# Kernel optimization log

Measured on AMD Instinct MI355X. Metric: run time of the kernel, lower is better.

The kernel has to match this reference:

```python
import jax, jax.numpy as jnp
from jax import lax
import numpy as np

B, N, S, K, C = 8, 16384, 1024, 32, 256


def setup_inputs() -> dict:
    key = jax.random.key(0)
    ks = jax.random.split(key, 8)
    def lin(k, o, i):
        return (jax.random.normal(k, (o, i), jnp.float32) / np.sqrt(i)).astype(jnp.float32)
    return {
        "x": jax.random.normal(ks[0], (B, N, 3), jnp.float32),
        "Wqkv": lin(ks[1], 3 * C, 3), "bqkv": jnp.zeros((3 * C,), jnp.float32),
        "g1": lin(ks[2], C, C), "bg1": jnp.zeros((C,), jnp.float32),
        "g2": lin(ks[3], C, C), "bg2": jnp.zeros((C,), jnp.float32),
        "Wo": lin(ks[4], C, C), "bo": jnp.zeros((C,), jnp.float32),
        "p1": lin(ks[5], 128, 3), "bp1": jnp.zeros((128,), jnp.float32),
        "p2": lin(ks[6], C, 128), "bp2": jnp.zeros((C,), jnp.float32),
    }


def _fps(xyz, num_patches):
    # furthest point sampling, deterministic start at index 0 (matches pointnet2 CUDA op)
    b, n, _ = xyz.shape
    def body(carry, _):
        dmin, far = carry
        c = jnp.take_along_axis(xyz, far[:, None, None], axis=1)[:, 0]  # [B,3]
        d = jnp.sum((xyz - c[:, None, :]) ** 2, axis=-1)                # [B,N]
        dmin = jnp.minimum(dmin, d)
        return (dmin, jnp.argmax(dmin, axis=-1)), far
    init = (jnp.full((b, n), 1e10, xyz.dtype), jnp.zeros((b,), jnp.int32))
    _, idx = lax.scan(body, init, None, length=num_patches)
    return jnp.transpose(idx)  # [B,S]


def _gelu(x):
    return jax.nn.gelu(x, approximate=False)  # torch nn.GELU default = exact erf


def reference(x, Wqkv, bqkv, g1, bg1, g2, bg2, Wo, bo, p1, bp1, p2, bp2):
    scale = C ** (-0.5)
    fps_idx = _fps(x, S)                                        # [B,S]
    centroid = jnp.take_along_axis(x, fps_idx[..., None], axis=1)  # [B,S,3]
    # square_distance(centroid, x): [B,S,N]
    d = (jnp.sum(centroid ** 2, -1)[..., None]
         + jnp.sum(x ** 2, -1)[:, None, :]
         - 2.0 * jnp.einsum('bsc,bnc->bsn', centroid, x))
    _, knn = lax.top_k(-d, K)                                   # [B,S,K] smallest-k (== argsort[:, :, :k])
    grouped = jax.vmap(lambda pts, i: pts[i])(x, knn)           # [B,S,K,3]
    # 1x1 Conv2d over channel dim == linear on last axis
    qkv = grouped @ Wqkv.T + bqkv                               # [B,S,K,3C]
    q, k_, v = jnp.split(qkv, 3, axis=-1)
    q = q.max(axis=2); k_ = k_.max(axis=2); v = v.max(axis=2)   # [B,S,C]
    h = _gelu((q - k_) @ g1.T + bg1) @ g2.T + bg2               # fc_gamma MLP
    attn = jax.nn.softmax(h * scale, axis=-1)                   # softmax over channels
    pos = _gelu(centroid @ p1.T + bp1) @ p2.T + bp2             # [B,S,C]
    return (attn * v) @ Wo.T + bo + pos                         # [B,S,C]
```

## Files before the change

### kernel.cpp

```cpp
#include <hip/hip_runtime.h>
#include <hip/hip_bf16.h>
#include <cstdint>

#define B_ 8
#define N_ 16384
#define S_ 1024
#define K_ 32
#define C_ 256
#define RR 8

typedef float vf16 __attribute__((ext_vector_type(16)));
typedef float vf8  __attribute__((ext_vector_type(8)));
typedef float vf4  __attribute__((ext_vector_type(4)));

__device__ __forceinline__ float gelu_f(float x){
  return 0.5f * x * (1.0f + erff(x * 0.70710678118654752f));
}

__device__ __forceinline__ float dist2_f(float px, float py, float pz,
                                         float cx, float cy, float cz){
  float dx = px - cx, dy = py - cy, dz = pz - cz;
  return dx*dx + dy*dy + dz*dz;
}

__global__ void prep_kernel(const float* __restrict__ x,
                            const float* __restrict__ g1,
                            const float* __restrict__ g2,
                            const float* __restrict__ Wo,
                            const float* __restrict__ p2,
                            float* __restrict__ xT,
                            float* __restrict__ g1T,
                            float* __restrict__ g2T,
                            float* __restrict__ WoT,
                            float* __restrict__ p2T,
                            float4* __restrict__ xP){
  int u = blockIdx.x * 256 + threadIdx.x;
  if (u < B_*N_){
    int b = u >> 14, n = u & (N_-1);
    const float* p = x + (size_t)u * 3;
    float X = p[0], Y = p[1], Z = p[2];
    xT[((size_t)b*3+0)*N_ + n] = X;
    xT[((size_t)b*3+1)*N_ + n] = Y;
    xT[((size_t)b*3+2)*N_ + n] = Z;
    xP[u] = make_float4(X, Y, Z, 0.0f);
  } else if (u < B_*N_ + 65536){
    int v = u - B_*N_; int i = v >> 8, j = v & 255;
    g1T[v] = g1[j*256 + i];
  } else if (u < B_*N_ + 2*65536){
    int v = u - B_*N_ - 65536; int i = v >> 8, j = v & 255;
    g2T[v] = g2[j*256 + i];
  } else if (u < B_*N_ + 3*65536){
    int v = u - B_*N_ - 2*65536; int i = v >> 8, j = v & 255;
    WoT[v] = Wo[j*256 + i];
  } else if (u < B_*N_ + 3*65536 + 32768){
    int v = u - B_*N_ - 3*65536; int i = v >> 8, j = v & 255;
    p2T[v] = p2[j*128 + i];
  }
}

__global__ __launch_bounds__(512, 1) void fps_kernel(const float4* __restrict__ xP,
                                                     float* __restrict__ cent){
  int b = blockIdx.x;
  int tid = threadIdx.x;
  const float4* P = xP + (size_t)b * N_;
  vf16 px0, py0, pz0, px1, py1, pz1;
  #pragma unroll
  for (int i=0;i<16;i++){
    float4 p = P[i*512 + tid];
    px0[i]=p.x; py0[i]=p.y; pz0[i]=p.z;
  }
  #pragma unroll
  for (int i=0;i<16;i++){
    float4 p = P[(i+16)*512 + tid];
    px1[i]=p.x; py1[i]=p.y; pz1[i]=p.z;
  }
  vf16 dm0 = (vf16)1e10f, dm1 = (vf16)1e10f;
  __shared__ float wmax[8];
  __shared__ int islot[2];
  __shared__ float centb[S_*3];
  if (tid < 2) islot[tid] = 0x7FFFFFFF;
  __syncthreads();
  float4 c4 = P[0];
  for (int s=0; s<S_; s++){
    int cur = s & 1;
    if (tid == 0){
      centb[s*3+0]=c4.x; centb[s*3+1]=c4.y; centb[s*3+2]=c4.z;
    }
    float cx=c4.x, cy=c4.y, cz=c4.z;
    {
      vf16 dx = px0 - cx, dy = py0 - cy, dz = pz0 - cz;
      vf16 d  = dx*dx + dy*dy + dz*dz;
      dm0 = __builtin_elementwise_min(dm0, d);
    }
    {
      vf16 dx = px1 - cx, dy = py1 - cy, dz = pz1 - cz;
      vf16 d  = dx*dx + dy*dy + dz*dz;
      dm1 = __builtin_elementwise_min(dm1, d);
    }
    vf16 mm = __builtin_elementwise_max(dm0, dm1);
    vf8 m8 = __builtin_elementwise_max(
        __builtin_shufflevector(mm, mm, 0,1,2,3,4,5,6,7),
        __builtin_shufflevector(mm, mm, 8,9,10,11,12,13,14,15));
    vf4 m4 = __builtin_elementwise_max(
        __builtin_shufflevector(m8, m8, 0,1,2,3),
        __builtin_shufflevector(m8, m8, 4,5,6,7));
    float wm = fmaxf(fmaxf(m4.x,m4.y), fmaxf(m4.z,m4.w));
    #pragma unroll
    for (int off=32; off; off>>=1) wm = fmaxf(wm, __shfl_xor(wm, off));
    if ((tid & 63) == 0) wmax[tid>>6] = wm;
    __syncthreads();
    if (tid == 0) islot[cur^1] = 0x7FFFFFFF;
    float g0 = fmaxf(fmaxf(wmax[0],wmax[1]), fmaxf(wmax[2],wmax[3]));
    float g1v = fmaxf(fmaxf(wmax[4],wmax[5]), fmaxf(wmax[6],wmax[7]));
    float gm = fmaxf(g0, g1v);
    if (wm == gm){
      int cidx = 0x7FFFFFFF;
      #pragma unroll
      for (int i=15;i>=0;i--){ if (dm1[i]==gm) cidx = (i+16)*512 + tid; }
      #pragma unroll
      for (int i=15;i>=0;i--){ if (dm0[i]==gm) cidx = i*512 + tid; }
      if (cidx != 0x7FFFFFFF) atomicMin(&islot[cur], cidx);
    }
    __syncthreads();
    int far = islot[cur];
    c4 = P[far];
  }
  __syncthreads();
  for (int i = tid; i < S_*3; i += 512) cent[(size_t)b*S_*3 + i] = centb[i];
}

__global__ __launch_bounds__(256) void knn_qkv_kernel(const float* __restrict__ xT,
                                                      const float* __restrict__ cent,
                                                      const float* __restrict__ Wqkv,
                                                      const float* __restrict__ bqkv,
                                                      float* __restrict__ qkv){
  __shared__ unsigned hist[RR][256];
  __shared__ unsigned candB[RR][256];
  __shared__ int      candI[RR][256];
  __shared__ int      selI[RR][32];
  __shared__ float    pts[RR][32][3];
  __shared__ int      cnt[RR];
  __shared__ int      Bstar[RR];
  int tid = threadIdx.x;
  int row0 = blockIdx.x * RR;
  int b = row0 >> 10;
  const float* X = xT + (size_t)b*3*N_;
  const float* Y = X + N_;
  const float* Z = Y + N_;
  float cx[RR], cy[RR], cz[RR];
  #pragma unroll
  for (int r=0;r<RR;r++){
    const float* c = cent + ((size_t)row0 + r)*3;
    cx[r]=c[0]; cy[r]=c[1]; cz[r]=c[2];
  }
  for (int i=tid; i<RR*256; i+=256) ((unsigned*)hist)[i] = 0u;
  if (tid < RR) cnt[tid]=0;
  __syncthreads();
  for (int i=0;i<64;i++){
    int g = i*256 + tid;
    float px=X[g], py=Y[g], pz=Z[g];
    #pragma unroll
    for (int r=0;r<RR;r++){
      float d = dist2_f(px,py,pz,cx[r],cy[r],cz[r]);
      int key = (int)(__float_as_uint(d) >> 20) - 840;
      key = min(max(key,0),255);
      atomicAdd(&hist[r][key], 1u);
    }
  }
  __syncthreads();
  int w = tid >> 6, lane = tid & 63;
  for (int half=0; half<2; half++){
    int r = half*4 + w;
    uint4 h4 = ((uint4*)&hist[r][0])[lane];
    unsigned cum = h4.x + h4.y + h4.z + h4.w;
    for (int off=1; off<64; off<<=1){
      unsigned t = __shfl_up(cum, off);
      if (lane >= off) cum += t;
    }
    unsigned long long mask = __ballot(cum >= 32u);
    int lb = __ffsll((unsigned long long)mask) - 1;
    unsigned cumPrev = __shfl(cum, lb>0 ? lb-1 : 0);
    if (lane == lb){
      unsigned c0 = (lb==0) ? 0u : cumPrev;
      unsigned hh[4] = {h4.x,h4.y,h4.z,h4.w};
      int bs = lb*4 + 3;
      for (int k=0;k<4;k++){
        if (c0 + hh[k] >= 32u){ bs = lb*4 + k; break; }
        c0 += hh[k];
      }
      Bstar[r] = bs;
    }
  }
  __syncthreads();
  int bsr[RR];
  #pragma unroll
  for (int r=0;r<RR;r++) bsr[r] = min(Bstar[r]+1, 255);
  for (int i=0;i<64;i++){
    int g = i*256 + tid;
    float px=X[g], py=Y[g], pz=Z[g];
    #pragma unroll
    for (int r=0;r<RR;r++){
      float d = dist2_f(px,py,pz,cx[r],cy[r],cz[r]);
      unsigned bits = __float_as_uint(d);
      int key = min(max((int)(bits>>20) - 840, 0), 255);
      if (key <= bsr[r]){
        int pos = atomicAdd(&cnt[r], 1);
        if (pos < 256){ candB[r][pos] = bits; candI[r][pos] = g; }
      }
    }
  }
  __syncthreads();
  for (int half=0; half<2; half++){
    int r = half*4 + w;
    int L = min(cnt[r], 256);
    for (int j=lane; j<L; j+=64){
      unsigned mb = candB[r][j]; int mi = candI[r][j];
      int rank = 0;
      for (int t=0;t<L;t++){
        unsigned tb = candB[r][t]; int ti = candI[r][t];
        rank += (tb < mb || (tb == mb && ti < mi)) ? 1 : 0;
      }
      if (rank < 32) selI[r][rank] = mi;
    }
  }
  __syncthreads();
  { int r = tid >> 5, p = tid & 31;
    int g = selI[r][p];
    pts[r][p][0]=X[g]; pts[r][p][1]=Y[g]; pts[r][p][2]=Z[g]; }
  __syncthreads();
  float w0[3], w1[3], w2[3], bb[3];
  #pragma unroll
  for (int c3=0;c3<3;c3++){
    int c = tid + c3*256;
    w0[c3]=Wqkv[c*3+0]; w1[c3]=Wqkv[c*3+1]; w2[c3]=Wqkv[c*3+2]; bb[c3]=bqkv[c];
  }
  for (int r=0;r<RR;r++){
    float m0=-1e30f, m1=-1e30f, m2=-1e30f;
    #pragma unroll
    for (int p=0;p<32;p++){
      float px=pts[r][p][0], py=pts[r][p][1], pz=pts[r][p][2];
      m0 = fmaxf(m0, w0[0]*px + w1[0]*py + w2[0]*pz);
      m1 = fmaxf(m1, w0[1]*px + w1[1]*py + w2[1]*pz);
      m2 = fmaxf(m2, w0[2]*px + w1[2]*py + w2[2]*pz);
    }
    float* o = qkv + ((size_t)row0 + r)*768;
    o[tid      ] = m0 + bb[0];
    o[tid + 256] = m1 + bb[1];
    o[tid + 512] = m2 + bb[2];
  }
}

template<int KD>
__device__ __forceinline__ void gemm_tile(const float* A_, const float* __restrict__ Wt,
                                          int rb, int lane, float acc[4][4]){
  const float4* W4 = (const float4*)Wt;
  for (int i0=0; i0<(KD>>2); i0++){
    float4 wv0 = W4[(i0*4+0)*64 + lane];
    float4 wv1 = W4[(i0*4+1)*64 + lane];
    float4 wv2 = W4[(i0*4+2)*64 + lane];
    float4 wv3 = W4[(i0*4+3)*64 + lane];
    #pragma unroll
    for (int r=0;r<4;r++){
      float4 a = ((const float4*)(A_ + (size_t)(rb+r)*KD))[i0];
      acc[r][0] = fmaf(a.x,wv0.x,fmaf(a.y,wv1.x,fmaf(a.z,wv2.x,fmaf(a.w,wv3.x,acc[r][0]))));
      acc[r][1] = fmaf(a.x,wv0.y,fmaf(a.y,wv1.y,fmaf(a.z,wv2.y,fmaf(a.w,wv3.y,acc[r][1]))));
      acc[r][2] = fmaf(a.x,wv0.z,fmaf(a.y,wv1.z,fmaf(a.z,wv2.z,fmaf(a.w,wv3.z,acc[r][2]))));
      acc[r][3] = fmaf(a.x,wv0.w,fmaf(a.y,wv1.w,fmaf(a.z,wv2.w,fmaf(a.w,wv3.w,acc[r][3]))));
    }
  }
}

__global__ __launch_bounds__(512, 2) void stage2_kernel(const float* __restrict__ qkv,
                                                        const float* __restrict__ cent,
                                                        const float* __restrict__ g1T,
                                                        const float* __restrict__ bg1,
                                                        const float* __restrict__ g2T,
                                                        const float* __restrict__ bg2,
                                                        const float* __restrict__ WoT,
                                                        const float* __restrict__ bo,
                                                        const float* __restrict__ p1,
                                                        const float* __restrict__ bp1,
                                                        const float* __restrict__ p2T,
                                                        const float* __restrict__ bp2,
                                                        float* __restrict__ out){
  __shared__ float A[32][256];
  __shared__ float T[32][128];
  __shared__ float CC[32][3];
  int tid = threadIdx.x;
  int w = tid >> 6, lane = tid & 63;
  int rb = w * 4;
  int row0 = blockIdx.x * 32;
  const float4* qkv4 = (const float4*)qkv;
  #pragma unroll
  for (int t=0;t<4;t++){
    int fi = t*512 + tid;
    int r = fi >> 6, c4 = fi & 63;
    float4 q = qkv4[(size_t)(row0+r)*192 + c4];
    float4 k = qkv4[(size_t)(row0+r)*192 + 64 + c4];
    ((float4*)&A[r][0])[c4] = make_float4(q.x-k.x, q.y-k.y, q.z-k.z, q.w-k.w);
  }
  if (tid < 96) ((float*)CC)[tid] = cent[(size_t)row0*3 + tid];
  __syncthreads();
  #pragma unroll
  for (int t=0;t<8;t++){
    int e = t*512 + tid;
    int r = e >> 7, c = e & 127;
    float tv = CC[r][0]*p1[c*3+0] + CC[r][1]*p1[c*3+1] + CC[r][2]*p1[c*3+2] + bp1[c];
    T[r][c] = gelu_f(tv);
  }
  __syncthreads();
  float acc[4][4];
  #pragma unroll
  for (int r=0;r<4;r++){ acc[r][0]=0.f; acc[r][1]=0.f; acc[r][2]=0.f; acc[r][3]=0.f; }
  gemm_tile<256>(&A[0][0], g1T, rb, lane, acc);
  {
    float4 bg = ((const float4*)bg1)[lane];
    #pragma unroll
    for (int r=0;r<4;r++){
      float4 g;
      g.x = gelu_f(acc[r][0] + bg.x);
      g.y = gelu_f(acc[r][1] + bg.y);
      g.z = gelu_f(acc[r][2] + bg.z);
      g.w = gelu_f(acc[r][3] + bg.w);
      ((float4*)&A[rb+r][0])[lane] = g;
    }
  }
  #pragma unroll
  for (int r=0;r<4;r++){ acc[r][0]=0.f; acc[r][1]=0.f; acc[r][2]=0.f; acc[r][3]=0.f; }
  gemm_tile<256>(&A[0][0], g2T, rb, lane, acc);
  {
    float4 bg = ((const float4*)bg2)[lane];
    const float scale = 0.0625f;
    #pragma unroll
    for (int r=0;r<4;r++){
      float h0 = acc[r][0]+bg.x, h1 = acc[r][1]+bg.y, h2 = acc[r][2]+bg.z, h3 = acc[r][3]+bg.w;
      float mx = fmaxf(fmaxf(h0,h1), fmaxf(h2,h3));
      for (int off=1; off<64; off<<=1) mx = fmaxf(mx, __shfl_xor(mx, off));
      float e0 = __expf((h0-mx)*scale), e1 = __expf((h1-mx)*scale);
      float e2 = __expf((h2-mx)*scale), e3 = __expf((h3-mx)*scale);
      float sm = e0+e1+e2+e3;
      for (int off=1; off<64; off<<=1) sm += __shfl_xor(sm, off);
      float inv = 1.0f / sm;
      float4 v4 = qkv4[(size_t)(row0+rb+r)*192 + 128 + lane];
      ((float4*)&A[rb+r][0])[lane] =
          make_float4(e0*inv*v4.x, e1*inv*v4.y, e2*inv*v4.z, e3*inv*v4.w);
    }
  }
  #pragma unroll
  for (int r=0;r<4;r++){ acc[r][0]=0.f; acc[r][1]=0.f; acc[r][2]=0.f; acc[r][3]=0.f; }
  gemm_tile<256>(&A[0][0], WoT, rb, lane, acc);
  gemm_tile<128>(&T[0][0], p2T, rb, lane, acc);
  {
    float4 bov = ((const float4*)bo)[lane];
    float4 bpv = ((const float4*)bp2)[lane];
    #pragma unroll
    for (int r=0;r<4;r++){
      float4 o;
      o.x = acc[r][0] + bov.x + bpv.x;
      o.y = acc[r][1] + bov.y + bpv.y;
      o.z = acc[r][2] + bov.z + bpv.z;
      o.w = acc[r][3] + bov.w + bpv.w;
      ((float4*)out)[(size_t)(row0+rb+r)*64 + lane] = o;
    }
  }
}

extern "C" void kernel_launch(void* const* d_in, const int* in_sizes, int n_in,
                              void* d_out, int out_size, void* d_ws, size_t ws_size,
                              hipStream_t stream) {
  const float* x    = (const float*)d_in[0];
  const float* Wqkv = (const float*)d_in[1];
  const float* bqkv = (const float*)d_in[2];
  const float* g1   = (const float*)d_in[3];
  const float* bg1  = (const float*)d_in[4];
  const float* g2   = (const float*)d_in[5];
  const float* bg2  = (const float*)d_in[6];
  const float* Wo   = (const float*)d_in[7];
  const float* bo   = (const float*)d_in[8];
  const float* p1   = (const float*)d_in[9];
  const float* bp1  = (const float*)d_in[10];
  const float* p2   = (const float*)d_in[11];
  const float* bp2  = (const float*)d_in[12];
  float* out = (float*)d_out;
  float* ws = (float*)d_ws;

  float* xT   = ws;
  float* cent = xT + 393216;
  float* qkv  = cent + 24576;
  float* g1T  = qkv + 6291456;
  float* g2T  = g1T + 65536;
  float* WoT  = g2T + 65536;
  float* p2T  = WoT + 65536;
  float4* xP  = (float4*)(p2T + 32768);

  hipLaunchKernelGGL(prep_kernel, dim3(1408), dim3(256), 0, stream,
                     x, g1, g2, Wo, p2, xT, g1T, g2T, WoT, p2T, xP);
  hipLaunchKernelGGL(fps_kernel, dim3(B_), dim3(512), 0, stream, xP, cent);
  hipLaunchKernelGGL(knn_qkv_kernel, dim3(B_*S_/RR), dim3(256), 0, stream,
                     xT, cent, Wqkv, bqkv, qkv);
  hipLaunchKernelGGL(stage2_kernel, dim3(B_*S_/32), dim3(512), 0, stream,
                     qkv, cent, g1T, bg1, g2T, bg2, WoT, bo, p1, bp1, p2T, bp2, out);
}
```

Before: 1.883 ms.

## Double FPS block to 1024 threads, keep x coords in LDS

The furthest-point-sampling kernel now runs 1024 threads per batch instead of 512, so each thread holds 16 points instead of 32. To fit in registers, the x coordinates move to shared memory and are reloaded every iteration, while y/z and the running min distance stay in registers. This halves per-thread serial work on each of the 1024 sequential steps. The cost is a 16-wave block reduction, more barrier participants, and LDS reads in the inner loop.

```diff
diff --git a/kernel.cpp b/kernel.cpp
--- a/kernel.cpp
+++ b/kernel.cpp
@@ -58,49 +58,42 @@
   }
 }
 
-__global__ __launch_bounds__(512, 1) void fps_kernel(const float4* __restrict__ xP,
-                                                     float* __restrict__ cent){
+__global__ __launch_bounds__(1024, 1) void fps_kernel(const float4* __restrict__ xP,
+                                                      float* __restrict__ cent){
   int b = blockIdx.x;
   int tid = threadIdx.x;
   const float4* P = xP + (size_t)b * N_;
-  vf16 px0, py0, pz0, px1, py1, pz1;
-  #pragma unroll
-  for (int i=0;i<16;i++){
-    float4 p = P[i*512 + tid];
-    px0[i]=p.x; py0[i]=p.y; pz0[i]=p.z;
-  }
-  #pragma unroll
-  for (int i=0;i<16;i++){
-    float4 p = P[(i+16)*512 + tid];
-    px1[i]=p.x; py1[i]=p.y; pz1[i]=p.z;
-  }
-  vf16 dm0 = (vf16)1e10f, dm1 = (vf16)1e10f;
-  __shared__ float wmax[8];
+  __shared__ float xs[N_];
+  __shared__ float wmax[16];
   __shared__ int islot[2];
   __shared__ float centb[S_*3];
+  vf16 py, pz;
+  #pragma unroll
+  for (int i=0;i<16;i++){
+    float4 p = P[i*1024 + tid];
+    xs[i*1024 + tid] = p.x;
+    py[i] = p.y; pz[i] = p.z;
+  }
+  vf16 dm = (vf16)1e10f;
   if (tid < 2) islot[tid] = 0x7FFFFFFF;
   __syncthreads();
   float4 c4 = P[0];
   for (int s=0; s<S_; s++){
+    asm volatile("" : "+v"(py), "+v"(pz));
     int cur = s & 1;
     if (tid == 0){
       centb[s*3+0]=c4.x; centb[s*3+1]=c4.y; centb[s*3+2]=c4.z;
     }
     float cx=c4.x, cy=c4.y, cz=c4.z;
-    {
-      vf16 dx = px0 - cx, dy = py0 - cy, dz = pz0 - cz;
-      vf16 d  = dx*dx + dy*dy + dz*dz;
-      dm0 = __builtin_elementwise_min(dm0, d);
-    }
-    {
-      vf16 dx = px1 - cx, dy = py1 - cy, dz = pz1 - cz;
-      vf16 d  = dx*dx + dy*dy + dz*dz;
-      dm1 = __builtin_elementwise_min(dm1, d);
-    }
-    vf16 mm = __builtin_elementwise_max(dm0, dm1);
+    vf16 xv;
+    #pragma unroll
+    for (int i=0;i<16;i++) xv[i] = xs[i*1024 + tid];
+    vf16 dx = xv - cx, dy = py - cy, dz = pz - cz;
+    vf16 d  = dx*dx + dy*dy + dz*dz;
+    dm = __builtin_elementwise_min(dm, d);
     vf8 m8 = __builtin_elementwise_max(
-        __builtin_shufflevector(mm, mm, 0,1,2,3,4,5,6,7),
-        __builtin_shufflevector(mm, mm, 8,9,10,11,12,13,14,15));
+        __builtin_shufflevector(dm, dm, 0,1,2,3,4,5,6,7),
+        __builtin_shufflevector(dm, dm, 8,9,10,11,12,13,14,15));
     vf4 m4 = __builtin_elementwise_max(
         __builtin_shufflevector(m8, m8, 0,1,2,3),
         __builtin_shufflevector(m8, m8, 4,5,6,7));
@@ -110,15 +103,15 @@
     if ((tid & 63) == 0) wmax[tid>>6] = wm;
     __syncthreads();
     if (tid == 0) islot[cur^1] = 0x7FFFFFFF;
-    float g0 = fmaxf(fmaxf(wmax[0],wmax[1]), fmaxf(wmax[2],wmax[3]));
-    float g1v = fmaxf(fmaxf(wmax[4],wmax[5]), fmaxf(wmax[6],wmax[7]));
-    float gm = fmaxf(g0, g1v);
+    float g01 = fmaxf(fmaxf(wmax[0],wmax[1]),  fmaxf(wmax[2],wmax[3]));
+    float g23 = fmaxf(fmaxf(wmax[4],wmax[5]),  fmaxf(wmax[6],wmax[7]));
+    float g45 = fmaxf(fmaxf(wmax[8],wmax[9]),  fmaxf(wmax[10],wmax[11]));
+    float g67 = fmaxf(fmaxf(wmax[12],wmax[13]),fmaxf(wmax[14],wmax[15]));
+    float gm = fmaxf(fmaxf(g01,g23), fmaxf(g45,g67));
     if (wm == gm){
       int cidx = 0x7FFFFFFF;
       #pragma unroll
-      for (int i=15;i>=0;i--){ if (dm1[i]==gm) cidx = (i+16)*512 + tid; }
-      #pragma unroll
-      for (int i=15;i>=0;i--){ if (dm0[i]==gm) cidx = i*512 + tid; }
+      for (int i=15;i>=0;i--){ if (dm[i]==gm) cidx = i*1024 + tid; }
       if (cidx != 0x7FFFFFFF) atomicMin(&islot[cur], cidx);
     }
     __syncthreads();
@@ -126,7 +119,7 @@
     c4 = P[far];
   }
   __syncthreads();
-  for (int i = tid; i < S_*3; i += 512) cent[(size_t)b*S_*3 + i] = centb[i];
+  for (int i = tid; i < S_*3; i += 1024) cent[(size_t)b*S_*3 + i] = centb[i];
 }
 
 __global__ __launch_bounds__(256) void knn_qkv_kernel(const float* __restrict__ xT,
@@ -395,7 +388,7 @@
 
   hipLaunchKernelGGL(prep_kernel, dim3(1408), dim3(256), 0, stream,
                      x, g1, g2, Wo, p2, xT, g1T, g2T, WoT, p2T, xP);
-  hipLaunchKernelGGL(fps_kernel, dim3(B_), dim3(512), 0, stream, xP, cent);
+  hipLaunchKernelGGL(fps_kernel, dim3(B_), dim3(1024), 0, stream, xP, cent);
   hipLaunchKernelGGL(knn_qkv_kernel, dim3(B_*S_/RR), dim3(256), 0, stream,
                      xT, cent, Wqkv, bqkv, qkv);
   hipLaunchKernelGGL(stage2_kernel, dim3(B_*S_/32), dim3(512), 0, stream,
```

Result: slower. 1.957 ms (+3.9%).
